# Optimization experiments

Hardware: AMD Instinct MI355X
Metric: run time of the kernel (lower is better)

The kernel has to match this reference:

```python
import jax, jax.numpy as jnp
import numpy as np

DIM = 2048
N_HEADS = 16
N_KV_HEADS = 4
HEAD_DIM = DIM // N_HEADS  # 128
N_REP = N_HEADS // N_KV_HEADS  # 4
BASE = 10000.0


def rotate_half(x):
    x1, x2 = jnp.split(x, 2, axis=-1)
    return jnp.concatenate((-x2, x1), axis=-1)


def rope_cos_sin(seq_len, dtype):
    inv_freq = 1.0 / (BASE ** (jnp.arange(0, HEAD_DIM, 2, dtype=jnp.float32) / HEAD_DIM))
    t = jnp.arange(seq_len, dtype=jnp.float32)
    freqs = jnp.outer(t, inv_freq)                      # [T, hd/2]
    emb = jnp.concatenate((freqs, freqs), axis=-1)      # [T, hd]
    return jnp.cos(emb).astype(dtype), jnp.sin(emb).astype(dtype)


def setup_inputs() -> dict:
    key = jax.random.key(0)
    ks = jax.random.split(key, 5)
    B, T = 2, 2048
    s_in = 1.0 / np.sqrt(DIM)
    x = jax.random.normal(ks[0], (B, T, DIM), dtype=jnp.float32)
    wq = jax.random.normal(ks[1], (DIM, N_HEADS * HEAD_DIM), dtype=jnp.float32) * s_in
    wk = jax.random.normal(ks[2], (DIM, N_KV_HEADS * HEAD_DIM), dtype=jnp.float32) * s_in
    wv = jax.random.normal(ks[3], (DIM, N_KV_HEADS * HEAD_DIM), dtype=jnp.float32) * s_in
    wo = jax.random.normal(ks[4], (DIM, DIM), dtype=jnp.float32) * s_in
    return {"x": x, "wq": wq, "wk": wk, "wv": wv, "wo": wo}


def reference(x, wq, wk, wv, wo):
    B, T, D = x.shape
    scale = HEAD_DIM ** -0.5
    # projections -> [B, H, T, hd]
    q = (x @ wq).reshape(B, T, N_HEADS, HEAD_DIM).transpose(0, 2, 1, 3)
    k = (x @ wk).reshape(B, T, N_KV_HEADS, HEAD_DIM).transpose(0, 2, 1, 3)
    v = (x @ wv).reshape(B, T, N_KV_HEADS, HEAD_DIM).transpose(0, 2, 1, 3)
    # RoPE
    cos, sin = rope_cos_sin(T, x.dtype)  # [T, hd]
    q = q * cos + rotate_half(q) * sin
    k = k * cos + rotate_half(k) * sin
    # GQA: group queries by kv head instead of repeating K/V
    qg = q.reshape(B, N_KV_HEADS, N_REP, T, HEAD_DIM)
    attn = jnp.einsum('bgrqd,bgkd->bgrqk', qg, k) * scale  # [B, G, R, T, T]
    causal = jnp.tril(jnp.ones((T, T), dtype=bool))
    attn = jnp.where(causal, attn, jnp.finfo(attn.dtype).min)
    attn = jax.nn.softmax(attn, axis=-1)
    out = jnp.einsum('bgrqk,bgkd->bgrqd', attn, v)  # [B, G, R, T, hd]
    out = out.reshape(B, N_HEADS, T, HEAD_DIM).transpose(0, 2, 1, 3).reshape(B, T, D)
    return out @ wo
```

## Files before the change

kernel.cpp:

```cpp
#include <hip/hip_runtime.h>
#include <hip/hip_bf16.h>

#define DIM 2048
#define T_SEQ 2048
#define B_SZ 2
#define NH 16
#define NKV 4
#define HD 128
#define KVDIM (NKV * HD)
#define M_ROWS (B_SZ * T_SEQ)
#define QKVN (DIM + 2 * KVDIM)
#define QBLK 128
#define KVBLK 64

typedef float f32x4 __attribute__((ext_vector_type(4)));
typedef __bf16 bf16x8 __attribute__((ext_vector_type(8)));
typedef unsigned short u16x8 __attribute__((ext_vector_type(8)));

static __device__ __forceinline__ float bf2f(unsigned short u) {
    unsigned v = ((unsigned)u) << 16;
    return __builtin_bit_cast(float, v);
}
static __device__ __forceinline__ unsigned short f2bf(float f) {
    __bf16 h = (__bf16)f;
    return __builtin_bit_cast(unsigned short, h);
}

static __device__ __forceinline__ void gload16(const void* g, void* l) {
    __builtin_amdgcn_global_load_lds((const __attribute__((address_space(1))) void*)g,
                                     (__attribute__((address_space(3))) void*)l, 16, 0, 0);
}

__global__ void cvt_f32_bf16(const float* __restrict__ src, unsigned short* __restrict__ dst, int n4) {
    int i = blockIdx.x * blockDim.x + threadIdx.x;
    if (i >= n4) return;
    float4 v = ((const float4*)src)[i];
    ushort4 o;
    o.x = f2bf(v.x); o.y = f2bf(v.y); o.z = f2bf(v.z); o.w = f2bf(v.w);
    ((ushort4*)dst)[i] = o;
}

__global__ void build_tab(float2* __restrict__ tab) {
    const int idx = blockIdx.x * 256 + threadIdx.x;
    if (idx >= T_SEQ * 64) return;
    const int tt = idx >> 6, i = idx & 63;
    const float inv = exp2f(-(float)i * (13.287712379549449f / 64.0f));
    const float ang = (float)tt * inv;
    tab[idx] = make_float2(cosf(ang), sinf(ang));
}

__global__ void transpose_cvt_qkv(const float* __restrict__ wq, const float* __restrict__ wk,
                                  const float* __restrict__ wv, unsigned short* __restrict__ dst) {
    __shared__ float tl[32][33];
    const int tx = threadIdx.x, ty = threadIdx.y;
    const int n0 = blockIdx.x * 32, k0 = blockIdx.y * 32;
    const float* src;
    int N, nn;
    if (n0 < DIM) { src = wq; N = DIM; nn = n0; }
    else if (n0 < DIM + KVDIM) { src = wk; N = KVDIM; nn = n0 - DIM; }
    else { src = wv; N = KVDIM; nn = n0 - DIM - KVDIM; }
#pragma unroll
    for (int i = 0; i < 4; ++i)
        tl[ty + i * 8][tx] = src[(size_t)(k0 + ty + i * 8) * N + nn + tx];
    __syncthreads();
#pragma unroll
    for (int i = 0; i < 4; ++i)
        dst[(size_t)(n0 + ty + i * 8) * DIM + k0 + tx] = f2bf(tl[tx][ty + i * 8]);
}

__global__ void transpose_cvt(const float* __restrict__ src, unsigned short* __restrict__ dst, int K, int N) {
    __shared__ float tl[32][33];
    const int tx = threadIdx.x, ty = threadIdx.y;
    const int n0 = blockIdx.x * 32, k0 = blockIdx.y * 32;
#pragma unroll
    for (int i = 0; i < 4; ++i)
        tl[ty + i * 8][tx] = src[(size_t)(k0 + ty + i * 8) * N + n0 + tx];
    __syncthreads();
#pragma unroll
    for (int i = 0; i < 4; ++i)
        dst[(size_t)(n0 + ty + i * 8) * K + k0 + tx] = f2bf(tl[tx][ty + i * 8]);
}

__global__ void transpose_v(const unsigned short* __restrict__ Vb, unsigned short* __restrict__ Vt) {
    __shared__ unsigned short tl[32][33];
    const int t0 = blockIdx.x * 32;
    const int d0 = blockIdx.y * 32;
    const int bg = blockIdx.z;
    const unsigned short* src = Vb + (size_t)bg * T_SEQ * HD;
    unsigned short* dst = Vt + (size_t)bg * T_SEQ * HD;
    const int tx = threadIdx.x, ty = threadIdx.y;
#pragma unroll
    for (int i = 0; i < 4; ++i)
        tl[ty + i * 8][tx] = src[(size_t)(t0 + ty + i * 8) * HD + d0 + tx];
    __syncthreads();
#pragma unroll
    for (int i = 0; i < 4; ++i)
        dst[(size_t)(d0 + ty + i * 8) * T_SEQ + t0 + tx] = tl[tx][ty + i * 8];
}

static __device__ __forceinline__ void store_out(float* p, float v) { *p = v; }
static __device__ __forceinline__ void store_out(unsigned short* p, float v) { *p = f2bf(v); }

template <typename OutT>
__global__ __launch_bounds__(512, 2) void gemm8(const unsigned short* __restrict__ A,
                                                const unsigned short* __restrict__ BT,
                                                OutT* __restrict__ C, int M, int N, int K, int Ntiles) {
    __shared__ __align__(16) unsigned short ldsA[2][2][256 * 32];
    __shared__ __align__(16) unsigned short ldsB[2][2][256 * 32];
    const int nwg = gridDim.x;
    const int f = blockIdx.x;
    const int swz = (f & 7) * (nwg >> 3) + (f >> 3);
    const int m0 = (swz / Ntiles) * 256, n0 = (swz % Ntiles) * 256;
    const int t = threadIdx.x;
    const int lane = t & 63, w = t >> 6;
    const int wr = w >> 2, wc = w & 3;
    const int grp = lane >> 4, c = lane & 15;
    const int nkt = K >> 6;

    const int Rs = t >> 2;
    const int cbs = ((t & 3) * 16) ^ ((Rs & 8) << 2);
    const char* Ag = (const char*)A + (size_t)(m0 + Rs) * (K * 2) + cbs;
    const char* Bg = (const char*)BT + (size_t)(n0 + Rs) * (K * 2) + cbs;
    const size_t rowstep = (size_t)128 * K * 2;

    auto stage = [&](int buf, int mat, int ks, int kt) {
        const char* g0 = (mat ? Bg : Ag) + kt * 128 + ks * 64;
        char* l = (mat ? (char*)&ldsB[buf][ks][0] : (char*)&ldsA[buf][ks][0]) + t * 16;
        gload16(g0, l);
        gload16(g0 + rowstep, l + 512 * 16);
    };
    auto rdA = [&](int buf, int ks, int fr) {
        const int R = wr * 128 + fr * 16 + c;
        return *(const bf16x8*)((const char*)&ldsA[buf][ks][0] + R * 64 + ((grp * 16) ^ ((R & 8) << 2)));
    };
    auto rdB = [&](int buf, int ks, int fc) {
        const int R = wc * 64 + fc * 16 + c;
        return *(const bf16x8*)((const char*)&ldsB[buf][ks][0] + R * 64 + ((grp * 16) ^ ((R & 8) << 2)));
    };

    f32x4 acc[8][4] = {};
    bf16x8 aF[8], bF0, bF1;

    stage(0, 0, 0, 0); stage(0, 1, 0, 0); stage(0, 0, 1, 0); stage(0, 1, 1, 0);
    stage(1, 0, 0, 1); stage(1, 1, 0, 1);
    asm volatile("s_waitcnt vmcnt(4)" ::: "memory");
    asm volatile("s_barrier" ::: "memory");

    for (int kt = 0; kt < nkt; ++kt) {
        const int buf = kt & 1;
#pragma unroll
        for (int fr = 0; fr < 8; ++fr) aF[fr] = rdA(buf, 0, fr);
        bF0 = rdB(buf, 0, 0); bF1 = rdB(buf, 0, 1);
        if (kt + 1 < nkt) stage(buf ^ 1, 0, 1, kt + 1);
        asm volatile("s_barrier" ::: "memory");
        __builtin_amdgcn_s_setprio(1);
#pragma unroll
        for (int fr = 0; fr < 8; ++fr) {
            acc[fr][0] = __builtin_amdgcn_mfma_f32_16x16x32_bf16(aF[fr], bF0, acc[fr][0], 0, 0, 0);
            acc[fr][1] = __builtin_amdgcn_mfma_f32_16x16x32_bf16(aF[fr], bF1, acc[fr][1], 0, 0, 0);
        }
        __builtin_amdgcn_s_setprio(0);
        asm volatile("s_barrier" ::: "memory");
        bF0 = rdB(buf, 0, 2); bF1 = rdB(buf, 0, 3);
        if (kt + 1 < nkt) stage(buf ^ 1, 1, 1, kt + 1);
        asm volatile("s_barrier" ::: "memory");
        __builtin_amdgcn_s_setprio(1);
#pragma unroll
        for (int fr = 0; fr < 8; ++fr) {
            acc[fr][2] = __builtin_amdgcn_mfma_f32_16x16x32_bf16(aF[fr], bF0, acc[fr][2], 0, 0, 0);
            acc[fr][3] = __builtin_amdgcn_mfma_f32_16x16x32_bf16(aF[fr], bF1, acc[fr][3], 0, 0, 0);
        }
        __builtin_amdgcn_s_setprio(0);
        asm volatile("s_barrier" ::: "memory");
#pragma unroll
        for (int fr = 0; fr < 8; ++fr) aF[fr] = rdA(buf, 1, fr);
        bF0 = rdB(buf, 1, 0); bF1 = rdB(buf, 1, 1);
        if (kt + 2 < nkt) stage(buf, 0, 0, kt + 2);
        asm volatile("s_barrier" ::: "memory");
        __builtin_amdgcn_s_setprio(1);
#pragma unroll
        for (int fr = 0; fr < 8; ++fr) {
            acc[fr][0] = __builtin_amdgcn_mfma_f32_16x16x32_bf16(aF[fr], bF0, acc[fr][0], 0, 0, 0);
            acc[fr][1] = __builtin_amdgcn_mfma_f32_16x16x32_bf16(aF[fr], bF1, acc[fr][1], 0, 0, 0);
        }
        __builtin_amdgcn_s_setprio(0);
        asm volatile("s_barrier" ::: "memory");
        bF0 = rdB(buf, 1, 2); bF1 = rdB(buf, 1, 3);
        if (kt + 2 < nkt) stage(buf, 1, 0, kt + 2);
        asm volatile("s_barrier" ::: "memory");
        __builtin_amdgcn_s_setprio(1);
#pragma unroll
        for (int fr = 0; fr < 8; ++fr) {
            acc[fr][2] = __builtin_amdgcn_mfma_f32_16x16x32_bf16(aF[fr], bF0, acc[fr][2], 0, 0, 0);
            acc[fr][3] = __builtin_amdgcn_mfma_f32_16x16x32_bf16(aF[fr], bF1, acc[fr][3], 0, 0, 0);
        }
        __builtin_amdgcn_s_setprio(0);
        asm volatile("s_waitcnt vmcnt(4)" ::: "memory");
        asm volatile("s_barrier" ::: "memory");
    }
#pragma unroll
    for (int fr = 0; fr < 8; ++fr)
#pragma unroll
        for (int fc = 0; fc < 4; ++fc)
#pragma unroll
            for (int rr = 0; rr < 4; ++rr) {
                const int row = m0 + wr * 128 + fr * 16 + grp * 4 + rr;
                const int col = n0 + wc * 64 + fc * 16 + c;
                store_out(&C[(size_t)row * N + col], acc[fr][fc][rr]);
            }
}

template <typename OutT>
__global__ __launch_bounds__(512, 1) void gemmwo(const unsigned short* __restrict__ A,
                                                 const unsigned short* __restrict__ BT,
                                                 OutT* __restrict__ C, int M, int N, int K, int Ntiles) {
    __shared__ __align__(16) unsigned short ldsA[2][2][256 * 32];
    __shared__ __align__(16) unsigned short ldsB[2][2][128 * 32];
    const int nwg = gridDim.x;
    const int f = blockIdx.x;
    const int swz = (f & 7) * (nwg >> 3) + (f >> 3);
    const int m0 = (swz / Ntiles) * 256, n0 = (swz % Ntiles) * 128;
    const int t = threadIdx.x;
    const int lane = t & 63, w = t >> 6;
    const int wr = w >> 2, wc = w & 3;
    const int grp = lane >> 4, c = lane & 15;
    const int nkt = K >> 6;

    const int Rs = t >> 2;
    const int cbs = ((t & 3) * 16) ^ ((Rs & 8) << 2);
    const char* Ag = (const char*)A + (size_t)(m0 + Rs) * (K * 2) + cbs;
    const char* Bg = (const char*)BT + (size_t)(n0 + Rs) * (K * 2) + cbs;
    const size_t rowstep = (size_t)128 * K * 2;

    auto stageA = [&](int buf, int ks, int kt) {
        const char* g0 = Ag + kt * 128 + ks * 64;
        char* l = (char*)&ldsA[buf][ks][0] + t * 16;
        gload16(g0, l);
        gload16(g0 + rowstep, l + 512 * 16);
    };
    auto stageB = [&](int buf, int ks, int kt) {
        gload16(Bg + kt * 128 + ks * 64, (char*)&ldsB[buf][ks][0] + t * 16);
    };
    auto rdA = [&](int buf, int ks, int fr) {
        const int R = wr * 128 + fr * 16 + c;
        return *(const bf16x8*)((const char*)&ldsA[buf][ks][0] + R * 64 + ((grp * 16) ^ ((R & 8) << 2)));
    };
    auto rdB = [&](int buf, int ks, int fc) {
        const int R = wc * 32 + fc * 16 + c;
        return *(const bf16x8*)((const char*)&ldsB[buf][ks][0] + R * 64 + ((grp * 16) ^ ((R & 8) << 2)));
    };

    f32x4 acc[8][2] = {};
    bf16x8 aF[8], bF0, bF1;

    stageA(0, 0, 0); stageB(0, 0, 0); stageA(0, 1, 0); stageB(0, 1, 0);
    stageA(1, 0, 1); stageB(1, 0, 1);
    asm volatile("s_waitcnt vmcnt(3)" ::: "memory");
    asm volatile("s_barrier" ::: "memory");

    for (int kt = 0; kt < nkt; ++kt) {
        const int buf = kt & 1;
#pragma unroll
        for (int fr = 0; fr < 8; ++fr) aF[fr] = rdA(buf, 0, fr);
        bF0 = rdB(buf, 0, 0); bF1 = rdB(buf, 0, 1);
        if (kt + 1 < nkt) { stageA(buf ^ 1, 1, kt + 1); stageB(buf ^ 1, 1, kt + 1); }
        asm volatile("s_barrier" ::: "memory");
        __builtin_amdgcn_s_setprio(1);
#pragma unroll
        for (int fr = 0; fr < 8; ++fr) {
            acc[fr][0] = __builtin_amdgcn_mfma_f32_16x16x32_bf16(aF[fr], bF0, acc[fr][0], 0, 0, 0);
            acc[fr][1] = __builtin_amdgcn_mfma_f32_16x16x32_bf16(aF[fr], bF1, acc[fr][1], 0, 0, 0);
        }
        __builtin_amdgcn_s_setprio(0);
        asm volatile("s_barrier" ::: "memory");
#pragma unroll
        for (int fr = 0; fr < 8; ++fr) aF[fr] = rdA(buf, 1, fr);
        bF0 = rdB(buf, 1, 0); bF1 = rdB(buf, 1, 1);
        if (kt + 2 < nkt) { stageA(buf, 0, kt + 2); stageB(buf, 0, kt + 2); }
        asm volatile("s_barrier" ::: "memory");
        __builtin_amdgcn_s_setprio(1);
#pragma unroll
        for (int fr = 0; fr < 8; ++fr) {
            acc[fr][0] = __builtin_amdgcn_mfma_f32_16x16x32_bf16(aF[fr], bF0, acc[fr][0], 0, 0, 0);
            acc[fr][1] = __builtin_amdgcn_mfma_f32_16x16x32_bf16(aF[fr], bF1, acc[fr][1], 0, 0, 0);
        }
        __builtin_amdgcn_s_setprio(0);
        if (kt + 2 < nkt) { asm volatile("s_waitcnt vmcnt(3)" ::: "memory"); }
        else              { asm volatile("s_waitcnt vmcnt(0)" ::: "memory"); }
        asm volatile("s_barrier" ::: "memory");
    }
#pragma unroll
    for (int fr = 0; fr < 8; ++fr)
#pragma unroll
        for (int fc = 0; fc < 2; ++fc)
#pragma unroll
            for (int rr = 0; rr < 4; ++rr) {
                const int row = m0 + wr * 128 + fr * 16 + grp * 4 + rr;
                const int col = n0 + wc * 32 + fc * 16 + c;
                store_out(&C[(size_t)row * N + col], acc[fr][fc][rr]);
            }
}

__global__ __launch_bounds__(256) void rope_pack(const unsigned short* __restrict__ qkv,
                                                 const float2* __restrict__ tab,
                                                 unsigned short* __restrict__ Qb,
                                                 unsigned short* __restrict__ Kb,
                                                 unsigned short* __restrict__ Vb) {
    const int bt = blockIdx.x;
    const int b = bt >> 11, tt = bt & 2047;
    __shared__ float cs[64], sn[64];
    const int tid = threadIdx.x;
    if (tid < 64) {
        float2 v = tab[tt * 64 + tid];
        cs[tid] = v.x;
        sn[tid] = v.y;
    }
    __syncthreads();
    const float qscale = 0.08838834764831845f * 1.4426950408889634f;
    const size_t src0 = (size_t)bt * QKVN;
#pragma unroll
    for (int iter = 0; iter < 4; ++iter) {
        const int idx = iter * 256 + tid;
        const int h = idx >> 6, i = idx & 63;
        const size_t src = src0 + h * HD;
        const float x1 = bf2f(qkv[src + i]), x2 = bf2f(qkv[src + i + 64]);
        const size_t dst = (((size_t)(b * NH + h)) * T_SEQ + tt) * HD;
        Qb[dst + i] = f2bf((x1 * cs[i] - x2 * sn[i]) * qscale);
        Qb[dst + i + 64] = f2bf((x2 * cs[i] + x1 * sn[i]) * qscale);
    }
    {
        const int gg = tid >> 6, i = tid & 63;
        const size_t src = src0 + DIM + gg * HD;
        const float x1 = bf2f(qkv[src + i]), x2 = bf2f(qkv[src + i + 64]);
        const size_t dst = (((size_t)(b * NKV + gg)) * T_SEQ + tt) * HD;
        Kb[dst + i] = f2bf(x1 * cs[i] - x2 * sn[i]);
        Kb[dst + i + 64] = f2bf(x2 * cs[i] + x1 * sn[i]);
    }
#pragma unroll
    for (int iter = 0; iter < 2; ++iter) {
        const int idx = iter * 256 + tid;
        const int gg = idx >> 7, i = idx & 127;
        const size_t dst = (((size_t)(b * NKV + gg)) * T_SEQ + tt) * HD;
        Vb[dst + i] = qkv[src0 + DIM + KVDIM + gg * HD + i];
    }
}

__global__ __launch_bounds__(512, 4) void attn_kernel(const unsigned short* __restrict__ Qb,
                                                      const unsigned short* __restrict__ Kb,
                                                      const unsigned short* __restrict__ Vt,
                                                      unsigned short* __restrict__ Ob) {
    __shared__ __align__(16) unsigned short Kl[2][KVBLK * HD];
    __shared__ __align__(16) unsigned short Vl[2][HD * KVBLK];
    const int bid = blockIdx.x;
    const int bh = bid & 31;
    const int qt = (T_SEQ / QBLK - 1) - (bid >> 5);
    const int b = bh >> 4, h = bh & 15;
    const int g = h >> 2;
    const int t = threadIdx.x, lane = t & 63, w = t >> 6;
    const int grp = lane >> 4, c = lane & 15;
    const int q0 = qt * QBLK;
    const int wq = q0 + w * 16;

    bf16x8 qf[4];
    {
        const size_t qbase = ((size_t)(b * NH + h) * T_SEQ + wq + c) * HD;
#pragma unroll
        for (int kk = 0; kk < 4; ++kk)
            qf[kk] = *(const bf16x8*)(Qb + qbase + kk * 32 + grp * 8);
    }
    const size_t kbase = (size_t)(b * NKV + g) * T_SEQ * HD;

    const char* kp[2];
    const char* vp[2];
#pragma unroll
    for (int i = 0; i < 2; ++i) {
        const int s = (i * 512 + t) * 16;
        const int rl = s >> 8, csw = s & 255;
        const int col = csw ^ ((rl & 7) << 4);
        const int rl32 = rl & 31;
        const int kvrow = (rl >> 5) * 32 + ((rl32 >> 2) & 3) * 8 + ((rl32 >> 4) & 1) * 4 + (rl32 & 3);
        kp[i] = (const char*)(Kb + kbase) + kvrow * (HD * 2) + col;
        const int d = s >> 7, csw2 = s & 127;
        const int kvb = csw2 ^ ((d & 7) << 4);
        vp[i] = (const char*)(Vt + kbase) + (size_t)d * (T_SEQ * 2) + kvb;
    }

    f32x4 o[8] = {};
    float l_run = 0.f;
    const int nkv = (q0 + QBLK) / KVBLK;

#pragma unroll
    for (int i = 0; i < 2; ++i) {
        gload16(kp[i], (char*)Kl[0] + (i * 512 + t) * 16);
        gload16(vp[i], (char*)Vl[0] + (i * 512 + t) * 16);
    }

    for (int kt = 0; kt < nkv; ++kt) {
        const int cur = kt & 1;
        __syncthreads();
        if (kt + 1 < nkv) {
#pragma unroll
            for (int i = 0; i < 2; ++i) {
                gload16(kp[i] + (size_t)(kt + 1) * (KVBLK * HD * 2), (char*)Kl[cur ^ 1] + (i * 512 + t) * 16);
                gload16(vp[i] + (size_t)(kt + 1) * (KVBLK * 2), (char*)Vl[cur ^ 1] + (i * 512 + t) * 16);
            }
        }
        const int kv0 = kt * KVBLK;
        if (kv0 > wq + 15) continue;
        f32x4 s4[4] = {};
        __builtin_amdgcn_s_setprio(1);
#pragma unroll
        for (int kvc = 0; kvc < 4; ++kvc) {
            const int row = kvc * 16 + c;
            bf16x8 kf[4];
#pragma unroll
            for (int kk = 0; kk < 4; ++kk)
                kf[kk] = *(const bf16x8*)((const char*)Kl[cur] + row * 256 +
                                          ((kk * 64 + grp * 16) ^ ((row & 7) << 4)));
#pragma unroll
            for (int kk = 0; kk < 4; ++kk)
                s4[kvc] = __builtin_amdgcn_mfma_f32_16x16x32_bf16(kf[kk], qf[kk], s4[kvc], 0, 0, 0);
        }
        __builtin_amdgcn_s_setprio(0);
        bf16x8 pb[2];
        if (kv0 + KVBLK - 1 > wq) {
#pragma unroll
            for (int kvc = 0; kvc < 4; ++kvc)
#pragma unroll
                for (int r = 0; r < 4; ++r) {
                    const int kvg = kv0 + (kvc >> 1) * 32 + grp * 8 + (kvc & 1) * 4 + r;
                    if (kvg > wq + c) s4[kvc][r] = -1e30f;
                }
        }
        float ls = 0.f;
#pragma unroll
        for (int kvc = 0; kvc < 4; ++kvc)
#pragma unroll
            for (int r = 0; r < 4; ++r) {
                const float pv = exp2f(s4[kvc][r]);
                pb[kvc >> 1][(kvc & 1) * 4 + r] = (__bf16)pv;
                ls += pv;
            }
        l_run += ls;
        __builtin_amdgcn_s_setprio(1);
#pragma unroll
        for (int ch = 0; ch < 2; ++ch) {
#pragma unroll
            for (int dt = 0; dt < 8; ++dt) {
                const int d = dt * 16 + c;
                const bf16x8 vf = *(const bf16x8*)((const char*)Vl[cur] + d * 128 +
                                                   ((ch * 64 + grp * 16) ^ ((d & 7) << 4)));
                o[dt] = __builtin_amdgcn_mfma_f32_16x16x32_bf16(pb[ch], vf, o[dt], 0, 0, 0);
            }
        }
        __builtin_amdgcn_s_setprio(0);
    }
    {
        float ls = l_run;
        ls += __shfl_xor(ls, 16);
        ls += __shfl_xor(ls, 32);
        float lo[4];
#pragma unroll
        for (int r = 0; r < 4; ++r) lo[r] = 1.0f / __shfl(ls, grp * 4 + r);
#pragma unroll
        for (int dt = 0; dt < 8; ++dt)
#pragma unroll
            for (int r = 0; r < 4; ++r) {
                const int trow = wq + grp * 4 + r;
                Ob[((size_t)(b * T_SEQ) + trow) * DIM + h * HD + dt * 16 + c] = f2bf(o[dt][r] * lo[r]);
            }
    }
}

extern "C" void kernel_launch(void* const* d_in, const int* in_sizes, int n_in,
                              void* d_out, int out_size, void* d_ws, size_t ws_size,
                              hipStream_t stream) {
    const float* x = (const float*)d_in[0];
    const float* wq = (const float*)d_in[1];
    const float* wk = (const float*)d_in[2];
    const float* wv = (const float*)d_in[3];
    const float* wo = (const float*)d_in[4];
    float* out = (float*)d_out;

    char* ws = (char*)d_ws;
    size_t off = 0;
    auto alloc = [&](size_t bytes) {
        char* p = ws + off;
        off = (off + bytes + 255) & ~(size_t)255;
        return p;
    };
    unsigned short* xb    = (unsigned short*)alloc((size_t)M_ROWS * DIM * 2);
    unsigned short* wqkvT = (unsigned short*)alloc((size_t)QKVN * DIM * 2);
    unsigned short* woT   = (unsigned short*)alloc((size_t)DIM * DIM * 2);
    unsigned short* qkv   = (unsigned short*)alloc((size_t)M_ROWS * QKVN * 2);
    unsigned short* Kb    = (unsigned short*)alloc((size_t)M_ROWS * KVDIM * 2);
    unsigned short* Vb    = (unsigned short*)alloc((size_t)M_ROWS * KVDIM * 2);
    float2*         tab   = (float2*)alloc((size_t)T_SEQ * 64 * sizeof(float2));
    unsigned short* Qb    = xb;
    unsigned short* Vt    = wqkvT;
    unsigned short* attnO = qkv;

    cvt_f32_bf16<<<(M_ROWS * DIM / 4 + 255) / 256, 256, 0, stream>>>(x, xb, M_ROWS * DIM / 4);
    build_tab<<<(T_SEQ * 64 + 255) / 256, 256, 0, stream>>>(tab);

    dim3 tb(32, 8);
    transpose_cvt_qkv<<<dim3(QKVN / 32, DIM / 32), tb, 0, stream>>>(wq, wk, wv, wqkvT);
    transpose_cvt<<<dim3(DIM / 32, DIM / 32), tb, 0, stream>>>(wo, woT, DIM, DIM);

    gemm8<unsigned short><<<(M_ROWS / 256) * (QKVN / 256), 512, 0, stream>>>(xb, wqkvT, qkv, M_ROWS, QKVN, DIM, QKVN / 256);

    rope_pack<<<M_ROWS, 256, 0, stream>>>(qkv, tab, Qb, Kb, Vb);
    transpose_v<<<dim3(T_SEQ / 32, HD / 32, B_SZ * NKV), tb, 0, stream>>>(Vb, Vt);

    attn_kernel<<<(B_SZ * NH) * (T_SEQ / QBLK), 512, 0, stream>>>(Qb, Kb, Vt, attnO);

    gemmwo<float><<<(M_ROWS / 256) * (DIM / 128), 512, 0, stream>>>(attnO, woT, out, M_ROWS, DIM, DIM, DIM / 128);
}
```

Measured before the change: 205.8 us.

## Split attention KV tile across wave pairs with LDS reduction and reorder q-tiles

Each pair of waves now shares 32 query rows, and each wave handles half of every 64-key tile. Each K fragment read from shared memory is reused for two query sub-tiles and each V fragment for two MFMAs. Partial outputs and row sums are combined through shared memory at the end, which reuses the K/V buffers and adds a small reduction array. Block-to-q-tile order changes from purely descending to half descending, then ascending. This changes the causal load balance across blocks and adds an extra barrier plus a reduction pass.

```diff
diff --git a/kernel.cpp b/kernel.cpp
--- a/kernel.cpp
+++ b/kernel.cpp
@@ -351,22 +351,26 @@
                                                       unsigned short* __restrict__ Ob) {
     __shared__ __align__(16) unsigned short Kl[2][KVBLK * HD];
     __shared__ __align__(16) unsigned short Vl[2][HD * KVBLK];
+    __shared__ float lred[4][2][64];
     const int bid = blockIdx.x;
     const int bh = bid & 31;
-    const int qt = (T_SEQ / QBLK - 1) - (bid >> 5);
+    const int idx = bid >> 5;
+    const int qt = (idx < 8) ? (15 - idx) : (idx - 8);
     const int b = bh >> 4, h = bh & 15;
     const int g = h >> 2;
     const int t = threadIdx.x, lane = t & 63, w = t >> 6;
+    const int wq = w >> 1, wkv = w & 1;
     const int grp = lane >> 4, c = lane & 15;
     const int q0 = qt * QBLK;
-    const int wq = q0 + w * 16;
-
-    bf16x8 qf[4];
-    {
-        const size_t qbase = ((size_t)(b * NH + h) * T_SEQ + wq + c) * HD;
+    const int qw = q0 + wq * 32;
+
+    bf16x8 qf[2][4];
+#pragma unroll
+    for (int qi = 0; qi < 2; ++qi) {
+        const size_t qbase = ((size_t)(b * NH + h) * T_SEQ + qw + qi * 16 + c) * HD;
 #pragma unroll
         for (int kk = 0; kk < 4; ++kk)
-            qf[kk] = *(const bf16x8*)(Qb + qbase + kk * 32 + grp * 8);
+            qf[qi][kk] = *(const bf16x8*)(Qb + qbase + kk * 32 + grp * 8);
     }
     const size_t kbase = (size_t)(b * NKV + g) * T_SEQ * HD;
 
@@ -381,12 +385,12 @@
         const int kvrow = (rl >> 5) * 32 + ((rl32 >> 2) & 3) * 8 + ((rl32 >> 4) & 1) * 4 + (rl32 & 3);
         kp[i] = (const char*)(Kb + kbase) + kvrow * (HD * 2) + col;
         const int d = s >> 7, csw2 = s & 127;
-        const int kvb = csw2 ^ ((d & 7) << 4);
-        vp[i] = (const char*)(Vt + kbase) + (size_t)d * (T_SEQ * 2) + kvb;
-    }
-
-    f32x4 o[8] = {};
-    float l_run = 0.f;
+        const int kvb2 = csw2 ^ ((d & 7) << 4);
+        vp[i] = (const char*)(Vt + kbase) + (size_t)d * (T_SEQ * 2) + kvb2;
+    }
+
+    f32x4 o[2][8] = {};
+    float l_run[2] = {0.f, 0.f};
     const int nkv = (q0 + QBLK) / KVBLK;
 
 #pragma unroll
@@ -406,69 +410,103 @@
             }
         }
         const int kv0 = kt * KVBLK;
-        if (kv0 > wq + 15) continue;
-        f32x4 s4[4] = {};
-        __builtin_amdgcn_s_setprio(1);
-#pragma unroll
-        for (int kvc = 0; kvc < 4; ++kvc) {
-            const int row = kvc * 16 + c;
+        const int kvb = kv0 + wkv * 32;
+        if (kvb > qw + 31) continue;
+        f32x4 s00 = {}, s01 = {}, s10 = {}, s11 = {};
+        __builtin_amdgcn_s_setprio(1);
+#pragma unroll
+        for (int j = 0; j < 2; ++j) {
+            const int row = wkv * 32 + j * 16 + c;
             bf16x8 kf[4];
 #pragma unroll
             for (int kk = 0; kk < 4; ++kk)
                 kf[kk] = *(const bf16x8*)((const char*)Kl[cur] + row * 256 +
                                           ((kk * 64 + grp * 16) ^ ((row & 7) << 4)));
 #pragma unroll
-            for (int kk = 0; kk < 4; ++kk)
-                s4[kvc] = __builtin_amdgcn_mfma_f32_16x16x32_bf16(kf[kk], qf[kk], s4[kvc], 0, 0, 0);
+            for (int kk = 0; kk < 4; ++kk) {
+                if (j == 0) {
+                    s00 = __builtin_amdgcn_mfma_f32_16x16x32_bf16(kf[kk], qf[0][kk], s00, 0, 0, 0);
+                    s10 = __builtin_amdgcn_mfma_f32_16x16x32_bf16(kf[kk], qf[1][kk], s10, 0, 0, 0);
+                } else {
+                    s01 = __builtin_amdgcn_mfma_f32_16x16x32_bf16(kf[kk], qf[0][kk], s01, 0, 0, 0);
+                    s11 = __builtin_amdgcn_mfma_f32_16x16x32_bf16(kf[kk], qf[1][kk], s11, 0, 0, 0);
+                }
+            }
         }
         __builtin_amdgcn_s_setprio(0);
         bf16x8 pb[2];
-        if (kv0 + KVBLK - 1 > wq) {
-#pragma unroll
-            for (int kvc = 0; kvc < 4; ++kvc)
+#pragma unroll
+        for (int qi = 0; qi < 2; ++qi) {
+            f32x4 sj0 = qi ? s10 : s00;
+            f32x4 sj1 = qi ? s11 : s01;
+            const int qrow = qw + qi * 16 + c;
+            if (kvb + 31 > qw + qi * 16) {
 #pragma unroll
                 for (int r = 0; r < 4; ++r) {
-                    const int kvg = kv0 + (kvc >> 1) * 32 + grp * 8 + (kvc & 1) * 4 + r;
-                    if (kvg > wq + c) s4[kvc][r] = -1e30f;
+                    const int base = kvb + grp * 8 + r;
+                    if (base > qrow) sj0[r] = -1e30f;
+                    if (base + 4 > qrow) sj1[r] = -1e30f;
                 }
-        }
-        float ls = 0.f;
-#pragma unroll
-        for (int kvc = 0; kvc < 4; ++kvc)
+            }
+            float ls = 0.f;
 #pragma unroll
             for (int r = 0; r < 4; ++r) {
-                const float pv = exp2f(s4[kvc][r]);
-                pb[kvc >> 1][(kvc & 1) * 4 + r] = (__bf16)pv;
-                ls += pv;
+                const float p0 = exp2f(sj0[r]);
+                const float p1 = exp2f(sj1[r]);
+                pb[qi][r] = (__bf16)p0;
+                pb[qi][4 + r] = (__bf16)p1;
+                ls += p0 + p1;
             }
-        l_run += ls;
-        __builtin_amdgcn_s_setprio(1);
-#pragma unroll
-        for (int ch = 0; ch < 2; ++ch) {
-#pragma unroll
-            for (int dt = 0; dt < 8; ++dt) {
-                const int d = dt * 16 + c;
-                const bf16x8 vf = *(const bf16x8*)((const char*)Vl[cur] + d * 128 +
-                                                   ((ch * 64 + grp * 16) ^ ((d & 7) << 4)));
-                o[dt] = __builtin_amdgcn_mfma_f32_16x16x32_bf16(pb[ch], vf, o[dt], 0, 0, 0);
-            }
-        }
-        __builtin_amdgcn_s_setprio(0);
-    }
-    {
-        float ls = l_run;
-        ls += __shfl_xor(ls, 16);
-        ls += __shfl_xor(ls, 32);
-        float lo[4];
-#pragma unroll
-        for (int r = 0; r < 4; ++r) lo[r] = 1.0f / __shfl(ls, grp * 4 + r);
-#pragma unroll
-        for (int dt = 0; dt < 8; ++dt)
-#pragma unroll
-            for (int r = 0; r < 4; ++r) {
-                const int trow = wq + grp * 4 + r;
-                Ob[((size_t)(b * T_SEQ) + trow) * DIM + h * HD + dt * 16 + c] = f2bf(o[dt][r] * lo[r]);
-            }
+            l_run[qi] += ls;
+        }
+        __builtin_amdgcn_s_setprio(1);
+#pragma unroll
+        for (int dt = 0; dt < 8; ++dt) {
+            const int d = dt * 16 + c;
+            const bf16x8 vf = *(const bf16x8*)((const char*)Vl[cur] + d * 128 +
+                                               ((wkv * 64 + grp * 16) ^ ((d & 7) << 4)));
+            o[0][dt] = __builtin_amdgcn_mfma_f32_16x16x32_bf16(pb[0], vf, o[0][dt], 0, 0, 0);
+            o[1][dt] = __builtin_amdgcn_mfma_f32_16x16x32_bf16(pb[1], vf, o[1][dt], 0, 0, 0);
+        }
+        __builtin_amdgcn_s_setprio(0);
+    }
+    __syncthreads();
+    float* obase = (wq < 2) ? ((float*)(char*)Kl + wq * 4096)
+                            : ((float*)(char*)Vl + (wq - 2) * 4096);
+    if (wkv) {
+#pragma unroll
+        for (int qi = 0; qi < 2; ++qi)
+#pragma unroll
+            for (int dt = 0; dt < 8; ++dt)
+                *(f32x4*)(obase + (qi * 8 + dt) * 256 + lane * 4) = o[qi][dt];
+        lred[wq][0][lane] = l_run[0];
+        lred[wq][1][lane] = l_run[1];
+    }
+    __syncthreads();
+    if (!wkv) {
+#pragma unroll
+        for (int qi = 0; qi < 2; ++qi)
+#pragma unroll
+            for (int dt = 0; dt < 8; ++dt)
+                o[qi][dt] += *(const f32x4*)(obase + (qi * 8 + dt) * 256 + lane * 4);
+        l_run[0] += lred[wq][0][lane];
+        l_run[1] += lred[wq][1][lane];
+#pragma unroll
+        for (int qi = 0; qi < 2; ++qi) {
+            float ls = l_run[qi];
+            ls += __shfl_xor(ls, 16);
+            ls += __shfl_xor(ls, 32);
+            float lo[4];
+#pragma unroll
+            for (int r = 0; r < 4; ++r) lo[r] = 1.0f / __shfl(ls, grp * 4 + r);
+#pragma unroll
+            for (int dt = 0; dt < 8; ++dt)
+#pragma unroll
+                for (int r = 0; r < 4; ++r) {
+                    const int trow = qw + qi * 16 + grp * 4 + r;
+                    Ob[((size_t)(b * T_SEQ) + trow) * DIM + h * HD + dt * 16 + c] = f2bf(o[qi][dt][r] * lo[r]);
+                }
+        }
     }
 }
 
```

Measured after the change: 323.5 us. 57.2% more time.
